# Kernel tuning notes

Measured on AMD Instinct MI355X. Metric: run time of the kernel, lower is better.

Reference implementation:

```python
import jax, jax.numpy as jnp
import numpy as np
import math

NUM_HEADS = 16
D_MODEL = 1024
LN_EPS = 1e-5


def _layer_norm(x, g, b):
    mu = jnp.mean(x, axis=-1, keepdims=True)
    var = jnp.mean((x - mu) ** 2, axis=-1, keepdims=True)
    return (x - mu) / jnp.sqrt(var + LN_EPS) * g + b


def setup_inputs() -> dict:
    key = jax.random.key(0)
    ks = jax.random.split(key, 12)
    B, H, W, d = 32, 16, 16, D_MODEL
    P, F = 64, 128
    s = 0.02
    return {
        "x": jax.random.normal(ks[0], (B, H, W, d), jnp.float32),
        "pattern_features": jax.random.normal(ks[1], (B, P, F), jnp.float32),
        "wq": jax.random.normal(ks[2], (d, d), jnp.float32) * s,
        "bq": jnp.zeros((d,), jnp.float32),
        "wk": jax.random.normal(ks[3], (d, d), jnp.float32) * s,
        "bk": jnp.zeros((d,), jnp.float32),
        "wv": jax.random.normal(ks[4], (d, d), jnp.float32) * s,
        "bv": jnp.zeros((d,), jnp.float32),
        "wo": jax.random.normal(ks[5], (d, d), jnp.float32) * s,
        "bo": jnp.zeros((d,), jnp.float32),
        "ln_g": jnp.ones((d,), jnp.float32),
        "ln_b": jnp.zeros((d,), jnp.float32),
    }


def reference(x, pattern_features, wq, bq, wk, bk, wv, bv, wo, bo, ln_g, ln_b):
    B, H, W, d = x.shape
    S = H * W
    nh = NUM_HEADS
    dk = d // nh
    x_seq = x.reshape(B, S, d)

    def proj(w, b):
        return (x_seq @ w.T + b).reshape(B, S, nh, dk).transpose(0, 2, 1, 3)  # (B,nh,S,dk)

    q, k, v = proj(wq, bq), proj(wk, bk), proj(wv, bv)
    scores = jnp.einsum("bhsd,bhtd->bhst", q, k) / math.sqrt(dk)  # (B,nh,S,S)

    # creative bias: diversity bonus on top-left min(S,64) block, same for all heads
    m = min(S, 64)
    sim = jnp.einsum("bpf,bqf->bpq", pattern_features, pattern_features)
    div = 1.0 - jax.nn.softmax(sim, axis=-1)  # (B,P,P)
    bias = jnp.zeros((B, nh, S, S), x.dtype)
    bias = bias.at[:, :, :m, :m].set(div[:, None, :m, :m] * 0.1)

    # faithful to torch: scores + bias.unsqueeze(0) -> rank-5 (1,B,nh,S,S)
    scores5 = scores[None] + bias[None]
    aw = jax.nn.softmax(scores5, axis=-1)
    attn = jnp.matmul(aw, v)  # (1,B,nh,S,dk) via broadcasting
    # faithful to torch transpose(1,2).view(B,S,d): row-major reshape of (1,nh,B,S,dk)
    attn = jnp.transpose(attn, (0, 2, 1, 3, 4)).reshape(B, S, d)

    out = attn @ wo.T + bo
    out = _layer_norm(out + x_seq, ln_g, ln_b)

    attention_weights = jax.nn.softmax(scores, axis=-1).mean(axis=1)  # (B,S,S)
    return out.reshape(B, H, W, d), attention_weights
```

## Files before the change

kernel.cpp:

```cpp
#include <hip/hip_runtime.h>

typedef unsigned short u16;
typedef unsigned int   u32;
typedef short bf16x8 __attribute__((ext_vector_type(8)));
typedef float f32x4  __attribute__((ext_vector_type(4)));

__device__ __forceinline__ float bf2f(u16 u){
  union { u32 u; float f; } c; c.u = ((u32)u) << 16; return c.f;
}
__device__ __forceinline__ u16 f2bf(float f){
  union { float f; u32 u; } c; c.f = f;
  u32 u = c.u + 0x7fffu + ((c.u >> 16) & 1u);
  return (u16)(u >> 16);
}

__device__ __forceinline__ void gload16(const u16* g, u16* l){
  __builtin_amdgcn_global_load_lds((const __attribute__((address_space(1))) u32*)g,
                                   (__attribute__((address_space(3))) u32*)l, 16, 0, 0);
}

__device__ __forceinline__ float waveRed(float v, int ismax){
  #pragma unroll
  for (int o = 32; o > 0; o >>= 1){
    float t = __shfl_xor(v, o, 64);
    v = ismax ? fmaxf(v, t) : (v + t);
  }
  return v;
}
__device__ __forceinline__ float blockRed(float v, int ismax, float* red, int tid){
  v = waveRed(v, ismax);
  __syncthreads();
  if ((tid & 63) == 0) red[tid >> 6] = v;
  __syncthreads();
  return ismax ? fmaxf(fmaxf(red[0], red[1]), fmaxf(red[2], red[3]))
               : (red[0] + red[1] + red[2] + red[3]);
}

__global__ __launch_bounds__(256)
void conv_x(const float* __restrict__ src, u16* __restrict__ dst){
  const size_t i = ((size_t)blockIdx.x * 256 + threadIdx.x) * 8;
  const float4 a = *(const float4*)(src + i);
  const float4 b = *(const float4*)(src + i + 4);
  uint4 o;
  o.x = (u32)f2bf(a.x) | ((u32)f2bf(a.y) << 16);
  o.y = (u32)f2bf(a.z) | ((u32)f2bf(a.w) << 16);
  o.z = (u32)f2bf(b.x) | ((u32)f2bf(b.y) << 16);
  o.w = (u32)f2bf(b.z) | ((u32)f2bf(b.w) << 16);
  *(uint4*)(dst + i) = o;
}

__global__ __launch_bounds__(256)
void conv_w4(const float* __restrict__ w0, const float* __restrict__ w1,
             const float* __restrict__ w2, const float* __restrict__ w3,
             u16* __restrict__ dst){
  const float* s = blockIdx.y == 0 ? w0 : (blockIdx.y == 1 ? w1 : (blockIdx.y == 2 ? w2 : w3));
  u16* d = dst + (size_t)blockIdx.y * 1048576;
  const size_t i = ((size_t)blockIdx.x * 256 + threadIdx.x) * 8;
  const float4 a = *(const float4*)(s + i);
  const float4 b = *(const float4*)(s + i + 4);
  uint4 o;
  o.x = (u32)f2bf(a.x) | ((u32)f2bf(a.y) << 16);
  o.y = (u32)f2bf(a.z) | ((u32)f2bf(a.w) << 16);
  o.z = (u32)f2bf(b.x) | ((u32)f2bf(b.y) << 16);
  o.w = (u32)f2bf(b.z) | ((u32)f2bf(b.w) << 16);
  *(uint4*)(d + i) = o;
}

__global__ __launch_bounds__(256)
void div_kernel(const float* __restrict__ pf, float* __restrict__ divp)
{
  __shared__ float pfs[64][129];
  __shared__ float svs[64][65];
  const int b = blockIdx.x;
  const int tid = threadIdx.x;
  const float* pb = pf + (size_t)b * 8192;
  for (int i = tid; i < 8192; i += 256) pfs[i >> 7][i & 127] = pb[i];
  __syncthreads();
  const int p = tid & 63, qg = tid >> 6;
  for (int qq = qg * 16; qq < qg * 16 + 16; ++qq){
    float a = 0.f;
    #pragma unroll 8
    for (int f = 0; f < 128; ++f) a += pfs[p][f] * pfs[qq][f];
    svs[p][qq] = a;
  }
  __syncthreads();
  if (tid < 64){
    float m = -1e30f;
    for (int qq = 0; qq < 64; ++qq) m = fmaxf(m, svs[tid][qq]);
    float s = 0.f;
    for (int qq = 0; qq < 64; ++qq){ const float e = __expf(svs[tid][qq] - m); svs[tid][qq] = e; s += e; }
    const float inv = 1.f / s;
    float* dr = divp + ((size_t)b * 64 + tid) * 64;
    for (int qq = 0; qq < 64; ++qq) dr[qq] = 0.1f * (1.f - svs[tid][qq] * inv);
  }
}

template<int MODE>
__global__ __launch_bounds__(256)
void gemm_lds(const u16* __restrict__ A, const u16* __restrict__ Wb,
              const float* __restrict__ bias0, const float* __restrict__ bias1,
              const float* __restrict__ bias2, void* __restrict__ outp)
{
  __shared__ u16 As[128 * 32];
  __shared__ u16 Bs[128 * 32];
  const int tid = threadIdx.x, lane = tid & 63, w = tid >> 6;
  const int wm = (w >> 1) * 64, wn = (w & 1) * 64;
  const int bm = blockIdx.x;
  int bn = blockIdx.y;
  const u16* Wp = Wb;
  const float* bias = bias0;
  float scale = 1.f;
  int wsel = 0;
  if (MODE == 0){
    wsel = bn >> 3; bn &= 7;
    Wp = Wb + (size_t)wsel * 1048576;
    bias = wsel == 0 ? bias0 : (wsel == 1 ? bias1 : bias2);
    if (wsel == 0) scale = 0.125f;
  }

  const f32x4 z = {0.f, 0.f, 0.f, 0.f};
  f32x4 acc[4][4];
  #pragma unroll
  for (int i = 0; i < 4; ++i)
    #pragma unroll
    for (int j = 0; j < 4; ++j) acc[i][j] = z;

  const int r4 = lane >> 2, c8 = (lane & 3) * 8;
  const int ca0 = w * 2, ca1 = w * 2 + 1;
  const u16* ga0 = A  + (size_t)(bm * 128 + ca0 * 16 + r4) * 1024 + c8;
  const u16* ga1 = A  + (size_t)(bm * 128 + ca1 * 16 + r4) * 1024 + c8;
  const u16* gb0 = Wp + (size_t)(bn * 128 + ca0 * 16 + r4) * 1024 + c8;
  const u16* gb1 = Wp + (size_t)(bn * 128 + ca1 * 16 + r4) * 1024 + c8;
  u16* la0 = As + ca0 * 512 + lane * 8;
  u16* la1 = As + ca1 * 512 + lane * 8;
  u16* lb0 = Bs + ca0 * 512 + lane * 8;
  u16* lb1 = Bs + ca1 * 512 + lane * 8;

  const int fr = lane & 15, q8 = (lane >> 4) * 8;
  for (int k0 = 0; k0 < 1024; k0 += 32){
    __syncthreads();
    gload16(ga0 + k0, la0);
    gload16(ga1 + k0, la1);
    gload16(gb0 + k0, lb0);
    gload16(gb1 + k0, lb1);
    __syncthreads();
    bf16x8 af[4], bfv[4];
    #pragma unroll
    for (int i = 0; i < 4; ++i) af[i]  = *(const bf16x8*)&As[(wm + i * 16 + fr) * 32 + q8];
    #pragma unroll
    for (int j = 0; j < 4; ++j) bfv[j] = *(const bf16x8*)&Bs[(wn + j * 16 + fr) * 32 + q8];
    #pragma unroll
    for (int i = 0; i < 4; ++i)
      #pragma unroll
      for (int j = 0; j < 4; ++j)
        acc[i][j] = __builtin_amdgcn_mfma_f32_16x16x32_bf16(af[i], bfv[j], acc[i][j], 0, 0, 0);
  }

  #pragma unroll
  for (int i = 0; i < 4; ++i){
    #pragma unroll
    for (int j = 0; j < 4; ++j){
      const int gr0 = bm * 128 + wm + i * 16 + ((lane >> 4) * 4);
      const int gc  = bn * 128 + wn + j * 16 + (lane & 15);
      const float bvv = bias[gc];
      #pragma unroll
      for (int r = 0; r < 4; ++r){
        const int gr = gr0 + r;
        const float val = (acc[i][j][r] + bvv) * scale;
        if (MODE == 0){
          const int b = gr >> 8, s = gr & 255, h = gc >> 6, kk = gc & 63;
          ((u16*)outp)[(size_t)wsel * 8388608 + (size_t)b * 262144 +
                       (size_t)h * 16384 + (size_t)s * 64 + kk] = f2bf(val);
        } else {
          ((float*)outp)[(size_t)gr * 1024 + gc] = val;
        }
      }
    }
  }
}

__global__ __launch_bounds__(256)
void attn_mfma(const u16* __restrict__ q, const u16* __restrict__ k,
               const u16* __restrict__ v, const float* __restrict__ divp,
               u16* __restrict__ attn_s)
{
  __shared__ u16 Vt[64][264];
  __shared__ u16 Ps[4][16][136];
  const int bh = blockIdx.x;
  const int b = bh >> 4, h = bh & 15;
  const int tid = threadIdx.x, lane = tid & 63, w = tid >> 6;
  const int quad = lane >> 4, l15 = lane & 15;
  const u16* kh = k + (size_t)bh * 16384;
  const u16* vh = v + (size_t)bh * 16384;
  const u16* qh = q + (size_t)bh * 16384;

  #pragma unroll
  for (int c = 0; c < 4; ++c){
    const int pidx = tid + c * 256;
    const int t2 = pidx & 127;
    const int n0 = (pidx >> 7) * 8;
    const uint4 a  = *(const uint4*)(vh + (2 * t2) * 64 + n0);
    const uint4 bb = *(const uint4*)(vh + (2 * t2 + 1) * 64 + n0);
    const u32 aa[4] = {a.x, a.y, a.z, a.w};
    const u32 bb4[4] = {bb.x, bb.y, bb.z, bb.w};
    #pragma unroll
    for (int j2 = 0; j2 < 4; ++j2){
      const u32 lo = aa[j2], hi = bb4[j2];
      *(u32*)&Vt[n0 + 2 * j2    ][2 * t2] = (lo & 0xffffu) | (hi << 16);
      *(u32*)&Vt[n0 + 2 * j2 + 1][2 * t2] = (lo >> 16) | (hi & 0xffff0000u);
    }
  }
  __syncthreads();

  const f32x4 z = {0.f, 0.f, 0.f, 0.f};
  const int bp = 2 * h + (b >> 4);
  for (int i = 0; i < 4; ++i){
    const int row0 = w * 64 + i * 16;
    const bf16x8 af0 = *(const bf16x8*)(qh + (size_t)(row0 + l15) * 64 + quad * 8);
    const bf16x8 af1 = *(const bf16x8*)(qh + (size_t)(row0 + l15) * 64 + 32 + quad * 8);
    f32x4 sc[16];
    #pragma unroll
    for (int ct = 0; ct < 16; ++ct){
      const bf16x8 b0 = *(const bf16x8*)(kh + (size_t)(ct * 16 + l15) * 64 + quad * 8);
      const bf16x8 b1 = *(const bf16x8*)(kh + (size_t)(ct * 16 + l15) * 64 + 32 + quad * 8);
      f32x4 a = __builtin_amdgcn_mfma_f32_16x16x32_bf16(af0, b0, z, 0, 0, 0);
      sc[ct]  = __builtin_amdgcn_mfma_f32_16x16x32_bf16(af1, b1, a, 0, 0, 0);
    }
    if (w == 0){
      const float* dv = divp + (size_t)b * 4096 + (size_t)(i * 16 + quad * 4) * 64 + l15;
      #pragma unroll
      for (int ct = 0; ct < 4; ++ct)
        #pragma unroll
        for (int rr = 0; rr < 4; ++rr)
          sc[ct][rr] += dv[rr * 64 + ct * 16];
    }
    float rs[4];
    #pragma unroll
    for (int rr = 0; rr < 4; ++rr){
      float m = sc[0][rr];
      #pragma unroll
      for (int ct = 1; ct < 16; ++ct) m = fmaxf(m, sc[ct][rr]);
      #pragma unroll
      for (int o = 1; o < 16; o <<= 1) m = fmaxf(m, __shfl_xor(m, o, 64));
      float s = 0.f;
      #pragma unroll
      for (int ct = 0; ct < 16; ++ct){
        const float e = __expf(sc[ct][rr] - m); sc[ct][rr] = e; s += e;
      }
      #pragma unroll
      for (int o = 1; o < 16; o <<= 1) s += __shfl_xor(s, o, 64);
      rs[rr] = 1.f / s;
    }
    f32x4 o4[4] = {z, z, z, z};
    #pragma unroll
    for (int half = 0; half < 2; ++half){
      #pragma unroll
      for (int ct = 0; ct < 8; ++ct)
        #pragma unroll
        for (int rr = 0; rr < 4; ++rr)
          Ps[w][quad * 4 + rr][ct * 16 + l15] = f2bf(sc[half * 8 + ct][rr] * rs[rr]);
      #pragma unroll
      for (int kc = 0; kc < 4; ++kc){
        const bf16x8 pa = *(const bf16x8*)&Ps[w][l15][kc * 32 + quad * 8];
        #pragma unroll
        for (int nt = 0; nt < 4; ++nt){
          const bf16x8 vb8 = *(const bf16x8*)&Vt[nt * 16 + l15][half * 128 + kc * 32 + quad * 8];
          o4[nt] = __builtin_amdgcn_mfma_f32_16x16x32_bf16(pa, vb8, o4[nt], 0, 0, 0);
        }
      }
    }
    const int sp = (b & 15) * 16 + (w * 4 + i);
    #pragma unroll
    for (int nt = 0; nt < 4; ++nt)
      #pragma unroll
      for (int rr = 0; rr < 4; ++rr){
        const int slo = quad * 4 + rr;
        const int cp = slo * 64 + nt * 16 + l15;
        attn_s[((size_t)bp * 256 + sp) * 1024 + cp] = f2bf(o4[nt][rr]);
      }
  }
}

__global__ __launch_bounds__(256)
void aw_kernel(const u16* __restrict__ q, const u16* __restrict__ k,
               float* __restrict__ aw)
{
  __shared__ float redm[16][4];
  __shared__ float reds[16][4];
  const int blk = blockIdx.x;
  const int b = blk >> 4, st = blk & 15;
  const int tid = threadIdx.x, lane = tid & 63, w = tid >> 6;
  const int quad = lane >> 4, l15 = lane & 15;
  const int rowb = st * 16;
  const f32x4 z = {0.f, 0.f, 0.f, 0.f};
  float awacc[4][4] = {};
  for (int h = 0; h < 16; ++h){
    const u16* kh = k + (((size_t)b * 16 + h) * 16384);
    const u16* qh = q + (((size_t)b * 16 + h) * 16384);
    const bf16x8 af0 = *(const bf16x8*)(qh + (size_t)(rowb + l15) * 64 + quad * 8);
    const bf16x8 af1 = *(const bf16x8*)(qh + (size_t)(rowb + l15) * 64 + 32 + quad * 8);
    f32x4 sc[4];
    #pragma unroll
    for (int j4 = 0; j4 < 4; ++j4){
      const int ct = w * 4 + j4;
      const bf16x8 b0 = *(const bf16x8*)(kh + (size_t)(ct * 16 + l15) * 64 + quad * 8);
      const bf16x8 b1 = *(const bf16x8*)(kh + (size_t)(ct * 16 + l15) * 64 + 32 + quad * 8);
      f32x4 a = __builtin_amdgcn_mfma_f32_16x16x32_bf16(af0, b0, z, 0, 0, 0);
      sc[j4]  = __builtin_amdgcn_mfma_f32_16x16x32_bf16(af1, b1, a, 0, 0, 0);
    }
    float pm[4];
    #pragma unroll
    for (int rr = 0; rr < 4; ++rr){
      float m = fmaxf(fmaxf(sc[0][rr], sc[1][rr]), fmaxf(sc[2][rr], sc[3][rr]));
      #pragma unroll
      for (int o = 1; o < 16; o <<= 1) m = fmaxf(m, __shfl_xor(m, o, 64));
      pm[rr] = m;
    }
    if (l15 == 0)
      #pragma unroll
      for (int rr = 0; rr < 4; ++rr) redm[quad * 4 + rr][w] = pm[rr];
    __syncthreads();
    float ps[4];
    #pragma unroll
    for (int rr = 0; rr < 4; ++rr){
      const int row = quad * 4 + rr;
      const float m = fmaxf(fmaxf(redm[row][0], redm[row][1]),
                            fmaxf(redm[row][2], redm[row][3]));
      float s = 0.f;
      #pragma unroll
      for (int j4 = 0; j4 < 4; ++j4){
        const float e = __expf(sc[j4][rr] - m); sc[j4][rr] = e; s += e;
      }
      #pragma unroll
      for (int o = 1; o < 16; o <<= 1) s += __shfl_xor(s, o, 64);
      ps[rr] = s;
    }
    if (l15 == 0)
      #pragma unroll
      for (int rr = 0; rr < 4; ++rr) reds[quad * 4 + rr][w] = ps[rr];
    __syncthreads();
    #pragma unroll
    for (int rr = 0; rr < 4; ++rr){
      const int row = quad * 4 + rr;
      const float inv = 1.f / (reds[row][0] + reds[row][1] + reds[row][2] + reds[row][3]);
      #pragma unroll
      for (int j4 = 0; j4 < 4; ++j4) awacc[j4][rr] += sc[j4][rr] * inv;
    }
  }
  const size_t base = (size_t)b * 65536;
  #pragma unroll
  for (int j4 = 0; j4 < 4; ++j4){
    const int col = (w * 4 + j4) * 16 + l15;
    #pragma unroll
    for (int rr = 0; rr < 4; ++rr){
      const int row = rowb + quad * 4 + rr;
      aw[base + (size_t)row * 256 + col] = awacc[j4][rr] * 0.0625f;
    }
  }
}

__global__ __launch_bounds__(256)
void ln_kernel(const float* __restrict__ y2, const float* __restrict__ x,
               const float* __restrict__ g, const float* __restrict__ bb,
               float* __restrict__ outp)
{
  __shared__ float red[4];
  const int r = blockIdx.x, tid = threadIdx.x;
  const float4 yv = ((const float4*)(y2 + (size_t)r * 1024))[tid];
  const float4 xv = ((const float4*)(x  + (size_t)r * 1024))[tid];
  const float v0 = yv.x + xv.x;
  const float v1 = yv.y + xv.y;
  const float v2 = yv.z + xv.z;
  const float v3 = yv.w + xv.w;
  const float ssum = blockRed(v0 + v1 + v2 + v3, 0, red, tid);
  const float mu = ssum * (1.f / 1024.f);
  const float d0 = v0 - mu, d1 = v1 - mu, d2 = v2 - mu, d3 = v3 - mu;
  const float sq = blockRed(d0 * d0 + d1 * d1 + d2 * d2 + d3 * d3, 0, red, tid);
  const float rstd = rsqrtf(sq * (1.f / 1024.f) + 1e-5f);
  const float4 gv = ((const float4*)g)[tid];
  const float4 bv = ((const float4*)bb)[tid];
  float4 o;
  o.x = d0 * rstd * gv.x + bv.x;
  o.y = d1 * rstd * gv.y + bv.y;
  o.z = d2 * rstd * gv.z + bv.z;
  o.w = d3 * rstd * gv.w + bv.w;
  ((float4*)(outp + (size_t)r * 1024))[tid] = o;
}

extern "C" void kernel_launch(void* const* d_in, const int* in_sizes, int n_in,
                              void* d_out, int out_size, void* d_ws, size_t ws_size,
                              hipStream_t stream)
{
  int ix = -1, ipf = -1, iw[4] = {-1,-1,-1,-1}, iv[6] = {-1,-1,-1,-1,-1,-1};
  int nw = 0, nv = 0;
  for (int i = 0; i < n_in; ++i){
    const int sz = in_sizes[i];
    if (sz == 8388608 && ix < 0) ix = i;
    else if (sz == 262144 && ipf < 0) ipf = i;
    else if (sz == 1048576 && nw < 4) iw[nw++] = i;
    else if (sz == 1024 && nv < 6) iv[nv++] = i;
  }
  if (ix < 0 || ipf < 0 || nw != 4 || nv != 6){
    ix = 0; ipf = 1; iw[0] = 2; iv[0] = 3; iw[1] = 4; iv[1] = 5;
    iw[2] = 6; iv[2] = 7; iw[3] = 8; iv[3] = 9; iv[4] = 10; iv[5] = 11;
  }

  const float* x   = (const float*)d_in[ix];
  const float* pf  = (const float*)d_in[ipf];
  const float* wq  = (const float*)d_in[iw[0]];
  const float* wk  = (const float*)d_in[iw[1]];
  const float* wv  = (const float*)d_in[iw[2]];
  const float* wo  = (const float*)d_in[iw[3]];
  const float* bq  = (const float*)d_in[iv[0]];
  const float* bk  = (const float*)d_in[iv[1]];
  const float* bv  = (const float*)d_in[iv[2]];
  const float* bo  = (const float*)d_in[iv[3]];
  const float* lng = (const float*)d_in[iv[4]];
  const float* lnb = (const float*)d_in[iv[5]];

  float* out0   = (float*)d_out;
  float* aw_out = out0 + 8388608;

  u16* x_bf = (u16*)d_out;
  u16* attn = x_bf + 8388608;
  u16* qkv    = (u16*)d_ws;
  float* divp = (float*)((char*)d_ws + (size_t)48 * 1048576);
  u16* warena = (u16*)((char*)d_ws + (size_t)49 * 1048576);
  float* y2   = (float*)d_ws;

  conv_x<<<4096, 256, 0, stream>>>(x, x_bf);
  conv_w4<<<dim3(512, 4), 256, 0, stream>>>(wq, wk, wv, wo, warena);
  div_kernel<<<32, 256, 0, stream>>>(pf, divp);

  gemm_lds<0><<<dim3(64, 24), 256, 0, stream>>>(x_bf, warena, bq, bk, bv, (void*)qkv);

  u16* qw = qkv, *kw = qkv + 8388608, *vw = qkv + 16777216;
  attn_mfma<<<512, 256, 0, stream>>>(qw, kw, vw, divp, attn);
  aw_kernel<<<512, 256, 0, stream>>>(qw, kw, aw_out);

  gemm_lds<1><<<dim3(64, 8), 256, 0, stream>>>(attn, warena + 3145728, bo, nullptr, nullptr, (void*)y2);
  ln_kernel<<<8192, 256, 0, stream>>>(y2, x, lng, lnb, out0);
}
```

Baseline: 331.7 us.

## Triple-buffer GEMM LDS tiles with async prefetch and XOR swizzle

The projection/output GEMM moves from a single-buffered LDS tile with two barriers per k-step to a three-stage ring buffer. Global-to-LDS loads are issued two steps ahead and guarded by explicit vmcnt waits, so only one barrier per iteration is needed. An XOR swizzle on the LDS column offsets is added to reduce bank conflicts on fragment reads, and MFMA priority is raised. This triples LDS use per block (24KB), which may limit occupancy, and relies on hand-placed waitcnt correctness.

```diff
diff --git a/kernel.cpp b/kernel.cpp
--- a/kernel.cpp
+++ b/kernel.cpp
@@ -96,13 +96,13 @@
 }
 
 template<int MODE>
-__global__ __launch_bounds__(256)
+__global__ __launch_bounds__(256, 3)
 void gemm_lds(const u16* __restrict__ A, const u16* __restrict__ Wb,
               const float* __restrict__ bias0, const float* __restrict__ bias1,
               const float* __restrict__ bias2, void* __restrict__ outp)
 {
-  __shared__ u16 As[128 * 32];
-  __shared__ u16 Bs[128 * 32];
+  __shared__ u16 As[3][4096];
+  __shared__ u16 Bs[3][4096];
   const int tid = threadIdx.x, lane = tid & 63, w = tid >> 6;
   const int wm = (w >> 1) * 64, wn = (w & 1) * 64;
   const int bm = blockIdx.x;
@@ -125,36 +125,73 @@
     #pragma unroll
     for (int j = 0; j < 4; ++j) acc[i][j] = z;
 
-  const int r4 = lane >> 2, c8 = (lane & 3) * 8;
+  const int r4  = lane >> 2;
+  const int c8s = (((lane & 3) ^ ((lane >> 3) & 3)) * 8);
   const int ca0 = w * 2, ca1 = w * 2 + 1;
-  const u16* ga0 = A  + (size_t)(bm * 128 + ca0 * 16 + r4) * 1024 + c8;
-  const u16* ga1 = A  + (size_t)(bm * 128 + ca1 * 16 + r4) * 1024 + c8;
-  const u16* gb0 = Wp + (size_t)(bn * 128 + ca0 * 16 + r4) * 1024 + c8;
-  const u16* gb1 = Wp + (size_t)(bn * 128 + ca1 * 16 + r4) * 1024 + c8;
-  u16* la0 = As + ca0 * 512 + lane * 8;
-  u16* la1 = As + ca1 * 512 + lane * 8;
-  u16* lb0 = Bs + ca0 * 512 + lane * 8;
-  u16* lb1 = Bs + ca1 * 512 + lane * 8;
-
-  const int fr = lane & 15, q8 = (lane >> 4) * 8;
-  for (int k0 = 0; k0 < 1024; k0 += 32){
-    __syncthreads();
-    gload16(ga0 + k0, la0);
-    gload16(ga1 + k0, la1);
-    gload16(gb0 + k0, lb0);
-    gload16(gb1 + k0, lb1);
-    __syncthreads();
+  const u16* gA0 = A  + (size_t)(bm * 128 + ca0 * 16 + r4) * 1024 + c8s;
+  const u16* gA1 = A  + (size_t)(bm * 128 + ca1 * 16 + r4) * 1024 + c8s;
+  const u16* gB0 = Wp + (size_t)(bn * 128 + ca0 * 16 + r4) * 1024 + c8s;
+  const u16* gB1 = Wp + (size_t)(bn * 128 + ca1 * 16 + r4) * 1024 + c8s;
+  const int lo0 = ca0 * 512 + lane * 8;
+  const int lo1 = ca1 * 512 + lane * 8;
+
+  const int fr = lane & 15, quad = lane >> 4;
+  int offA[4], offB[4];
+  #pragma unroll
+  for (int i = 0; i < 4; ++i){
+    const int r = wm + i * 16 + fr;
+    offA[i] = r * 32 + ((quad ^ ((r >> 1) & 3)) * 8);
+  }
+  #pragma unroll
+  for (int j = 0; j < 4; ++j){
+    const int r = wn + j * 16 + fr;
+    offB[j] = r * 32 + ((quad ^ ((r >> 1) & 3)) * 8);
+  }
+
+#define STG(s, kk) \
+    gload16(gA0 + (kk), &As[s][lo0]); \
+    gload16(gA1 + (kk), &As[s][lo1]); \
+    gload16(gB0 + (kk), &Bs[s][lo0]); \
+    gload16(gB1 + (kk), &Bs[s][lo1]);
+
+  STG(0, 0)
+  STG(1, 32)
+  asm volatile("s_waitcnt vmcnt(4)" ::: "memory");
+  __builtin_amdgcn_sched_barrier(0);
+  __builtin_amdgcn_s_barrier();
+  asm volatile("" ::: "memory");
+  __builtin_amdgcn_sched_barrier(0);
+
+  int slot = 0;
+  #pragma unroll 1
+  for (int t = 0; t < 32; ++t){
+    const int s2 = slot < 1 ? 2 : slot - 1;
+    if (t < 30){ STG(s2, (t + 2) * 32) }
+    const u16* as_ = As[slot];
+    const u16* bs_ = Bs[slot];
     bf16x8 af[4], bfv[4];
     #pragma unroll
-    for (int i = 0; i < 4; ++i) af[i]  = *(const bf16x8*)&As[(wm + i * 16 + fr) * 32 + q8];
-    #pragma unroll
-    for (int j = 0; j < 4; ++j) bfv[j] = *(const bf16x8*)&Bs[(wn + j * 16 + fr) * 32 + q8];
+    for (int i = 0; i < 4; ++i) af[i]  = *(const bf16x8*)&as_[offA[i]];
+    #pragma unroll
+    for (int j = 0; j < 4; ++j) bfv[j] = *(const bf16x8*)&bs_[offB[j]];
+    __builtin_amdgcn_s_setprio(1);
     #pragma unroll
     for (int i = 0; i < 4; ++i)
       #pragma unroll
       for (int j = 0; j < 4; ++j)
         acc[i][j] = __builtin_amdgcn_mfma_f32_16x16x32_bf16(af[i], bfv[j], acc[i][j], 0, 0, 0);
-  }
+    __builtin_amdgcn_s_setprio(0);
+    if (t < 30)       { asm volatile("s_waitcnt vmcnt(4)" ::: "memory"); }
+    else if (t == 30) { asm volatile("s_waitcnt vmcnt(0)" ::: "memory"); }
+    if (t < 31){
+      __builtin_amdgcn_sched_barrier(0);
+      __builtin_amdgcn_s_barrier();
+      asm volatile("" ::: "memory");
+      __builtin_amdgcn_sched_barrier(0);
+    }
+    slot = slot == 2 ? 0 : slot + 1;
+  }
+#undef STG
 
   #pragma unroll
   for (int i = 0; i < 4; ++i){
```

After: 330.2 us. Within noise of the previous version (-0.4%).
